# Performance work log

Hardware: AMD Instinct MI355X
Metric: run time of the kernel (lower is better)

The kernel has to match this reference:

```python
import jax, jax.numpy as jnp
import numpy as np

B = 131072
IN_C = 10
N = 512
HEAD_DIMS = [N, 128, 64, 32, 16, 1]
N_HEADS = 8


def _init_linear(key, fan_in, fan_out, batch=None):
    kw, kb = jax.random.split(key)
    shape_w = (fan_in, fan_out) if batch is None else (batch, fan_in, fan_out)
    shape_b = (fan_out,) if batch is None else (batch, fan_out)
    lim = 1.0 / np.sqrt(fan_in)
    W = jax.random.uniform(kw, shape_w, jnp.float32, -lim, lim)
    b = jax.random.uniform(kb, shape_b, jnp.float32, -lim, lim)
    return W, b


def setup_inputs() -> dict:
    key = jax.random.key(0)
    keys = jax.random.split(key, 10)
    x = jax.random.normal(keys[0], (B, IN_C), jnp.float32)
    W1, b1 = _init_linear(keys[1], 3 * IN_C, N)
    W2, b2 = _init_linear(keys[2], N, N)
    W3, b3 = _init_linear(keys[3], N, N - 3 * IN_C)
    W4, b4 = _init_linear(keys[4], N, N)
    inp = {"x": x, "W1": W1, "b1": b1, "W2": W2, "b2": b2,
           "W3": W3, "b3": b3, "W4": W4, "b4": b4}
    # 8 identical-shaped heads stacked into grouped weights [8, in, out]
    for i in range(5):
        HW, Hb = _init_linear(keys[5 + i], HEAD_DIMS[i], HEAD_DIMS[i + 1], batch=N_HEADS)
        inp[f"HW{i+1}"] = HW
        inp[f"Hb{i+1}"] = Hb
    return inp


def reference(x, W1, b1, W2, b2, W3, b3, W4, b4,
              HW1, Hb1, HW2, Hb2, HW3, Hb3, HW4, Hb4, HW5, Hb5):
    # backbone
    x_skip = jnp.concatenate([x, jnp.sin(x), jnp.cos(x)], axis=-1)  # [B, 3c]
    h = jax.nn.relu(x_skip @ W1 + b1)
    h = jax.nn.relu(h @ W2 + b2)
    h = h @ W3 + b3                                                  # [B, N-3c]
    h = jax.nn.relu(jnp.concatenate([h, x_skip], axis=1))            # [B, N]
    h = h @ W4 + b4  # NOTE: original discards the relu here (no assignment)
    # 8 heads as grouped batched GEMMs: y[g] = head_g(h)
    y = jax.nn.relu(jnp.einsum('bd,gde->gbe', h, HW1) + Hb1[:, None, :])
    y = jax.nn.relu(jnp.einsum('gbd,gde->gbe', y, HW2) + Hb2[:, None, :])
    y = jax.nn.relu(jnp.einsum('gbd,gde->gbe', y, HW3) + Hb3[:, None, :])
    y = jax.nn.relu(jnp.einsum('gbd,gde->gbe', y, HW4) + Hb4[:, None, :])
    y = jnp.einsum('gbd,gde->gbe', y, HW5) + Hb5[:, None, :]         # [8, B, 1]
    return jnp.transpose(y[..., 0])                                  # [B, 8]
```

## Files before the change

kernel.cpp:

```cpp
#include <hip/hip_runtime.h>
#include <hip/hip_bf16.h>

typedef short s16x8 __attribute__((ext_vector_type(8)));
typedef float f32x4 __attribute__((ext_vector_type(4)));
typedef unsigned short u16;
typedef unsigned int u32;

#define TB 64
#define NTHREADS 512

#define P_L1 0
#define P_L2 16384
#define P_L3 278528
#define P_L4 540672
#define P_H1 802816
#define P_H2 1327104
#define P_H3 1392640
#define P_H4 1409024
#define P_TOT 1413120

#define H_OFF   0
#define XS_OFF  65536
#define Y1_OFF  73728
#define LDS_BYTES 139264

__device__ __forceinline__ u16 f2bf(float v) {
  __hip_bfloat16 b = __float2bfloat16(v);
  return __builtin_bit_cast(u16, b);
}
__device__ __forceinline__ float bf2f(u16 u) {
  u32 x = ((u32)u) << 16;
  return __builtin_bit_cast(float, x);
}

template<int FN>
__device__ __forceinline__ void loadB(s16x8 (&b)[FN], const char* unit,
                                      int nCols, int bColBase, int kg, int l15) {
#pragma unroll
  for (int fj = 0; fj < FN; ++fj) {
    const int n = bColBase + fj * 16 + l15;
    b[fj] = *reinterpret_cast<const s16x8*>(unit + (kg * nCols + n) * 16);
  }
}

template<int FM, int FN>
__device__ __forceinline__ void mfma_step(
    const char* lds, int aOff, int aRB, int kByte, int mBase, int l15,
    const s16x8 (&b)[FN], f32x4 (&acc)[FM][FN]) {
  s16x8 a[FM];
#pragma unroll
  for (int fi = 0; fi < FM; ++fi) {
    const int m = mBase + fi * 16 + l15;
    a[fi] = *reinterpret_cast<const s16x8*>(
        lds + aOff + m * aRB + (kByte ^ (((m & 7) << 4) & (aRB - 1))));
  }
#pragma unroll
  for (int fi = 0; fi < FM; ++fi)
#pragma unroll
    for (int fj = 0; fj < FN; ++fj)
      acc[fi][fj] = __builtin_amdgcn_mfma_f32_16x16x32_bf16(a[fi], b[fj], acc[fi][fj], 0, 0, 0);
}

template<int FM, int FN, int KSTEPS>
__device__ __forceinline__ void gemm_reg(
    const char* lds, int aOff, int aRB, int aColBase, int mBase,
    const char* bGlob, int unitStride, int nCols, int bColBase,
    int kg, int l15, f32x4 (&acc)[FM][FN]) {
#pragma unroll
  for (int i = 0; i < FM; ++i)
#pragma unroll
    for (int j = 0; j < FN; ++j) { f32x4 z = {0.f,0.f,0.f,0.f}; acc[i][j] = z; }
  s16x8 bA[FN], bB[FN];
  loadB<FN>(bA, bGlob, nCols, bColBase, kg, l15);
#pragma unroll
  for (int ks = 0; ks < KSTEPS; ks += 2) {
    if (ks + 1 < KSTEPS)
      loadB<FN>(bB, bGlob + (size_t)(ks + 1) * unitStride, nCols, bColBase, kg, l15);
    mfma_step<FM, FN>(lds, aOff, aRB, (aColBase + ks * 32 + kg * 8) * 2,
                      mBase, l15, bA, acc);
    if (ks + 1 < KSTEPS) {
      if (ks + 2 < KSTEPS)
        loadB<FN>(bA, bGlob + (size_t)(ks + 2) * unitStride, nCols, bColBase, kg, l15);
      mfma_step<FM, FN>(lds, aOff, aRB, (aColBase + (ks + 1) * 32 + kg * 8) * 2,
                        mBase, l15, bB, acc);
    }
  }
}

__device__ __forceinline__ void epi_bb(char* lds, const f32x4 (&acc)[4][4],
    const float* bias, int biasLim, bool relu, bool concatXS, int tid)
{
  const int lane = tid & 63;
  const int l15 = lane & 15, rgrp = lane >> 4;
  const int wid = tid >> 6;
#pragma unroll
  for (int fj = 0; fj < 4; ++fj) {
    const int gc = wid * 64 + fj * 16 + l15;
    const float bv = (gc < biasLim) ? bias[gc] : 0.f;
#pragma unroll
    for (int fi = 0; fi < 4; ++fi) {
#pragma unroll
      for (int r = 0; r < 4; ++r) {
        const int m = fi * 16 + rgrp * 4 + r;
        float v = acc[fi][fj][r] + bv;
        if (relu) v = fmaxf(v, 0.f);
        u16 hv = f2bf(v);
        if (concatXS && gc >= 482) {
          const int c2 = gc - 482;
          const float xv = bf2f(*reinterpret_cast<const u16*>(
              lds + XS_OFF + m * 128 + ((c2 * 2) ^ ((m & 7) << 4))));
          hv = f2bf(fmaxf(xv, 0.f));
        }
        *reinterpret_cast<u16*>(lds + H_OFF + m * 1024 + ((gc * 2) ^ ((m & 7) << 4))) = hv;
      }
    }
  }
}

__global__ __launch_bounds__(256)
void prep_weights(const float* __restrict__ W1, const float* __restrict__ W2,
                  const float* __restrict__ W3, const float* __restrict__ W4,
                  const float* __restrict__ HW1, const float* __restrict__ HW2,
                  const float* __restrict__ HW3, const float* __restrict__ HW4,
                  u16* __restrict__ wp)
{
  for (int idx = blockIdx.x * blockDim.x + threadIdx.x; idx < P_TOT;
       idx += gridDim.x * blockDim.x) {
    float v;
    if (idx < P_L2) {
      const int e = idx;
      const int kg = e >> 12, n = (e >> 3) & 511, j = e & 7;
      const int k = kg * 8 + j;
      v = (k < 30) ? W1[k * 512 + n] : 0.f;
    } else if (idx < P_L3) {
      const int e = idx - P_L2;
      const int u = e >> 14, r = e & 16383;
      const int kg = r >> 12, n = (r >> 3) & 511, j = r & 7;
      const int k = u * 32 + kg * 8 + j;
      v = W2[k * 512 + n];
    } else if (idx < P_L4) {
      const int e = idx - P_L3;
      const int u = e >> 14, r = e & 16383;
      const int kg = r >> 12, n = (r >> 3) & 511, j = r & 7;
      const int k = u * 32 + kg * 8 + j;
      v = (n < 482) ? W3[k * 482 + n] : 0.f;
    } else if (idx < P_H1) {
      const int e = idx - P_L4;
      const int u = e >> 14, r = e & 16383;
      const int kg = r >> 12, n = (r >> 3) & 511, j = r & 7;
      const int k = u * 32 + kg * 8 + j;
      v = W4[k * 512 + n];
    } else if (idx < P_H2) {
      const int e = idx - P_H1;
      const int p = e >> 17, r = e & 131071;
      const int u = r >> 13, q = r & 8191;
      const int kg = q >> 11, n = (q >> 3) & 255, j = q & 7;
      const int k = u * 32 + kg * 8 + j;
      const int g = 2 * p + (n >> 7), col = n & 127;
      v = HW1[((size_t)g * 512 + k) * 128 + col];
    } else if (idx < P_H3) {
      const int e = idx - P_H2;
      const int p = e >> 14, r = e & 16383;
      const int u = r >> 12, q = r & 4095;
      const int kg = q >> 10, n = (q >> 3) & 127, j = q & 7;
      const int k = u * 32 + kg * 8 + j;
      const int g = 2 * p + (n >> 6), col = n & 63;
      v = HW2[((size_t)g * 128 + k) * 64 + col];
    } else if (idx < P_H4) {
      const int e = idx - P_H3;
      const int p = e >> 12, r = e & 4095;
      const int u = r >> 11, q = r & 2047;
      const int kg = q >> 9, n = (q >> 3) & 63, j = q & 7;
      const int k = u * 32 + kg * 8 + j;
      const int g = 2 * p + (n >> 5), col = n & 31;
      v = HW3[((size_t)g * 64 + k) * 32 + col];
    } else {
      const int e = idx - P_H4;
      const int p = e >> 10, q = e & 1023;
      const int kg = q >> 8, n = (q >> 3) & 31, j = q & 7;
      const int k = kg * 8 + j;
      const int g = 2 * p + (n >> 4), col = n & 15;
      v = HW4[((size_t)g * 32 + k) * 16 + col];
    }
    wp[idx] = f2bf(v);
  }
}

__global__ __launch_bounds__(NTHREADS, 2)
void fused_mlp(const float* __restrict__ x, const u16* __restrict__ wp,
               const float* __restrict__ b1, const float* __restrict__ b2,
               const float* __restrict__ b3, const float* __restrict__ b4,
               const float* __restrict__ Hb1, const float* __restrict__ Hb2,
               const float* __restrict__ Hb3, const float* __restrict__ Hb4,
               const float* __restrict__ hw5, const float* __restrict__ Hb5,
               float* __restrict__ out)
{
  extern __shared__ char lds[];
  const int tid = threadIdx.x;
  const int lane = tid & 63;
  const int l15 = lane & 15;
  const int rgrp = lane >> 4;
  const int kg = lane >> 4;
  const int wid = tid >> 6;
  const int row0 = blockIdx.x * TB;
  const char* wpB = reinterpret_cast<const char*>(wp);

  for (int i = tid; i < TB * 10; i += NTHREADS) {
    const int r = i / 10, c = i % 10;
    const float xv = x[(size_t)(row0 + r) * 10 + c];
    const int sw = (r & 7) << 4;
    char* rowp = lds + XS_OFF + r * 128;
    *reinterpret_cast<u16*>(rowp + ((c * 2) ^ sw)) = f2bf(xv);
    *reinterpret_cast<u16*>(rowp + (((c + 10) * 2) ^ sw)) = f2bf(__sinf(xv));
    *reinterpret_cast<u16*>(rowp + (((c + 20) * 2) ^ sw)) = f2bf(__cosf(xv));
  }
  for (int i = tid; i < TB * 2; i += NTHREADS) {
    const int r = i >> 1, c = 30 + (i & 1);
    *reinterpret_cast<u16*>(lds + XS_OFF + r * 128 + ((c * 2) ^ ((r & 7) << 4))) = 0;
  }
  __syncthreads();

  {
    f32x4 acc[4][4];
    gemm_reg<4, 4, 1>(lds, XS_OFF, 128, 0, 0,
                      wpB + (size_t)P_L1 * 2, 8192, 512, wid * 64, kg, l15, acc);
    epi_bb(lds, acc, b1, 512, true, false, tid);
    __syncthreads();
  }
  {
    f32x4 acc[4][4];
    gemm_reg<4, 4, 16>(lds, H_OFF, 1024, 0, 0,
                       wpB + (size_t)P_L2 * 2, 32768, 512, wid * 64, kg, l15, acc);
    __syncthreads();
    epi_bb(lds, acc, b2, 512, true, false, tid);
    __syncthreads();
  }
  {
    f32x4 acc[4][4];
    gemm_reg<4, 4, 16>(lds, H_OFF, 1024, 0, 0,
                       wpB + (size_t)P_L3 * 2, 32768, 512, wid * 64, kg, l15, acc);
    __syncthreads();
    epi_bb(lds, acc, b3, 482, true, true, tid);
    __syncthreads();
  }
  {
    f32x4 acc[4][4];
    gemm_reg<4, 4, 16>(lds, H_OFF, 1024, 0, 0,
                       wpB + (size_t)P_L4 * 2, 32768, 512, wid * 64, kg, l15, acc);
    __syncthreads();
    epi_bb(lds, acc, b4, 512, false, false, tid);
    __syncthreads();
  }

  {
    const int half = wid & 1;
    const int mB = half * 32;
    for (int grp = 0; grp < 2; ++grp) {
      const int g = grp * 4 + (wid >> 1);
      const int pair = g >> 1, side = g & 1;
      const int y1o = Y1_OFF + (g & 3) * 16384;
      const int scrOff = y1o + half * 8192;
      char* scr = lds + scrOff;

#pragma unroll
      for (int pass = 0; pass < 2; ++pass) {
        f32x4 acc[2][4];
        gemm_reg<2, 4, 16>(lds, H_OFF, 1024, 0, mB,
                           wpB + (size_t)P_H1 * 2 + (size_t)pair * 262144, 16384, 256,
                           side * 128 + pass * 64, kg, l15, acc);
#pragma unroll
        for (int fj = 0; fj < 4; ++fj) {
          const int c = pass * 64 + fj * 16 + l15;
          const float bv = Hb1[g * 128 + c];
#pragma unroll
          for (int fi = 0; fi < 2; ++fi)
#pragma unroll
            for (int r = 0; r < 4; ++r) {
              const int m = mB + fi * 16 + rgrp * 4 + r;
              const float v = fmaxf(acc[fi][fj][r] + bv, 0.f);
              *reinterpret_cast<u16*>(lds + y1o + m * 256 + ((c * 2) ^ ((m & 7) << 4))) = f2bf(v);
            }
        }
      }
      {
        f32x4 a2[2][4];
        gemm_reg<2, 4, 4>(lds, scrOff, 256, 0, 0,
                          wpB + (size_t)P_H2 * 2 + (size_t)pair * 32768, 8192, 128,
                          side * 64, kg, l15, a2);
#pragma unroll
        for (int fj = 0; fj < 4; ++fj) {
          const int c = fj * 16 + l15;
          const float bv = Hb2[g * 64 + c];
#pragma unroll
          for (int fi = 0; fi < 2; ++fi)
#pragma unroll
            for (int r = 0; r < 4; ++r) {
              const int rl = fi * 16 + rgrp * 4 + r;
              const float v = fmaxf(a2[fi][fj][r] + bv, 0.f);
              *reinterpret_cast<u16*>(scr + rl * 256 + ((c * 2) ^ ((rl & 7) << 4))) = f2bf(v);
            }
        }
      }
      {
        f32x4 a3[2][2];
        gemm_reg<2, 2, 2>(lds, scrOff, 256, 0, 0,
                          wpB + (size_t)P_H3 * 2 + (size_t)pair * 8192, 4096, 64,
                          side * 32, kg, l15, a3);
#pragma unroll
        for (int fj = 0; fj < 2; ++fj) {
          const int c = fj * 16 + l15;
          const float bv = Hb3[g * 32 + c];
#pragma unroll
          for (int fi = 0; fi < 2; ++fi)
#pragma unroll
            for (int r = 0; r < 4; ++r) {
              const int rl = fi * 16 + rgrp * 4 + r;
              const float v = fmaxf(a3[fi][fj][r] + bv, 0.f);
              *reinterpret_cast<u16*>(scr + rl * 256 + ((c * 2) ^ ((rl & 7) << 4))) = f2bf(v);
            }
        }
      }
      {
        f32x4 a4[2][1];
        gemm_reg<2, 1, 1>(lds, scrOff, 256, 0, 0,
                          wpB + (size_t)P_H4 * 2 + (size_t)pair * 2048, 2048, 32,
                          side * 16, kg, l15, a4);
        const int c = l15;
        const float bv = Hb4[g * 16 + c];
#pragma unroll
        for (int fi = 0; fi < 2; ++fi)
#pragma unroll
          for (int r = 0; r < 4; ++r) {
            const int rl = fi * 16 + rgrp * 4 + r;
            const float v = fmaxf(a4[fi][0][r] + bv, 0.f);
            *reinterpret_cast<u16*>(scr + rl * 256 + ((c * 2) ^ ((rl & 7) << 4))) = f2bf(v);
          }
      }
      {
        const int r = lane & 31, kh = lane >> 5;
        const s16x8 y4v = *reinterpret_cast<const s16x8*>(
            scr + r * 256 + ((kh * 16) ^ ((r & 7) << 4)));
        float partial = 0.f;
#pragma unroll
        for (int j = 0; j < 8; ++j)
          partial += bf2f((u16)y4v[j]) * hw5[g * 16 + kh * 8 + j];
        partial += __shfl_xor(partial, 32, 64);
        if (kh == 0)
          out[(size_t)(row0 + mB + r) * 8 + g] = Hb5[g] + partial;
      }
    }
  }
}

extern "C" void kernel_launch(void* const* d_in, const int* in_sizes, int n_in,
                              void* d_out, int out_size, void* d_ws, size_t ws_size,
                              hipStream_t stream) {
  (void)in_sizes; (void)n_in; (void)out_size; (void)ws_size;
  const float* x   = (const float*)d_in[0];
  const float* W1  = (const float*)d_in[1];
  const float* b1  = (const float*)d_in[2];
  const float* W2  = (const float*)d_in[3];
  const float* b2  = (const float*)d_in[4];
  const float* W3  = (const float*)d_in[5];
  const float* b3  = (const float*)d_in[6];
  const float* W4  = (const float*)d_in[7];
  const float* b4  = (const float*)d_in[8];
  const float* HW1 = (const float*)d_in[9];
  const float* Hb1 = (const float*)d_in[10];
  const float* HW2 = (const float*)d_in[11];
  const float* Hb2 = (const float*)d_in[12];
  const float* HW3 = (const float*)d_in[13];
  const float* Hb3 = (const float*)d_in[14];
  const float* HW4 = (const float*)d_in[15];
  const float* Hb4 = (const float*)d_in[16];
  const float* HW5 = (const float*)d_in[17];
  const float* Hb5 = (const float*)d_in[18];
  float* out = (float*)d_out;
  u16* wp = (u16*)d_ws;

  prep_weights<<<2048, 256, 0, stream>>>(W1, W2, W3, W4, HW1, HW2, HW3, HW4, wp);

  hipFuncSetAttribute((const void*)fused_mlp,
                      hipFuncAttributeMaxDynamicSharedMemorySize, LDS_BYTES);
  fused_mlp<<<131072 / TB, NTHREADS, LDS_BYTES, stream>>>(
      x, wp, b1, b2, b3, b4, Hb1, Hb2, Hb3, Hb4, HW5, Hb5, out);
}
```

Baseline: 427.7 us.

## Double-buffer activations in LDS and prefetch next layer's first weight tile

```diff
diff --git a/kernel.cpp b/kernel.cpp
--- a/kernel.cpp
+++ b/kernel.cpp
@@ -19,9 +19,9 @@
 #define P_H4 1409024
 #define P_TOT 1413120
 
-#define H_OFF   0
-#define XS_OFF  65536
-#define Y1_OFF  73728
+#define BUF0   0
+#define XS_OFF 65536
+#define BUF1   73728
 #define LDS_BYTES 139264
 
 __device__ __forceinline__ u16 f2bf(float v) {
@@ -62,16 +62,15 @@
 }
 
 template<int FM, int FN, int KSTEPS>
-__device__ __forceinline__ void gemm_reg(
+__device__ __forceinline__ void gemm_pre(
     const char* lds, int aOff, int aRB, int aColBase, int mBase,
     const char* bGlob, int unitStride, int nCols, int bColBase,
-    int kg, int l15, f32x4 (&acc)[FM][FN]) {
+    int kg, int l15, f32x4 (&acc)[FM][FN], s16x8 (&bA)[FN]) {
 #pragma unroll
   for (int i = 0; i < FM; ++i)
 #pragma unroll
     for (int j = 0; j < FN; ++j) { f32x4 z = {0.f,0.f,0.f,0.f}; acc[i][j] = z; }
-  s16x8 bA[FN], bB[FN];
-  loadB<FN>(bA, bGlob, nCols, bColBase, kg, l15);
+  s16x8 bB[FN];
 #pragma unroll
   for (int ks = 0; ks < KSTEPS; ks += 2) {
     if (ks + 1 < KSTEPS)
@@ -87,8 +86,19 @@
   }
 }
 
+template<int FM, int FN, int KSTEPS>
+__device__ __forceinline__ void gemm_reg(
+    const char* lds, int aOff, int aRB, int aColBase, int mBase,
+    const char* bGlob, int unitStride, int nCols, int bColBase,
+    int kg, int l15, f32x4 (&acc)[FM][FN]) {
+  s16x8 bA[FN];
+  loadB<FN>(bA, bGlob, nCols, bColBase, kg, l15);
+  gemm_pre<FM, FN, KSTEPS>(lds, aOff, aRB, aColBase, mBase, bGlob, unitStride,
+                           nCols, bColBase, kg, l15, acc, bA);
+}
+
 __device__ __forceinline__ void epi_bb(char* lds, const f32x4 (&acc)[4][4],
-    const float* bias, int biasLim, bool relu, bool concatXS, int tid)
+    int outOff, const float* bias, int biasLim, bool relu, bool concatXS, int tid)
 {
   const int lane = tid & 63;
   const int l15 = lane & 15, rgrp = lane >> 4;
@@ -111,7 +121,7 @@
               lds + XS_OFF + m * 128 + ((c2 * 2) ^ ((m & 7) << 4))));
           hv = f2bf(fmaxf(xv, 0.f));
         }
-        *reinterpret_cast<u16*>(lds + H_OFF + m * 1024 + ((gc * 2) ^ ((m & 7) << 4))) = hv;
+        *reinterpret_cast<u16*>(lds + outOff + m * 1024 + ((gc * 2) ^ ((m & 7) << 4))) = hv;
       }
     }
   }
@@ -205,6 +215,9 @@
   const int row0 = blockIdx.x * TB;
   const char* wpB = reinterpret_cast<const char*>(wp);
 
+  s16x8 bPre[4];
+  loadB<4>(bPre, wpB + (size_t)P_L1 * 2, 512, wid * 64, kg, l15);
+
   for (int i = tid; i < TB * 10; i += NTHREADS) {
     const int r = i / 10, c = i % 10;
     const float xv = x[(size_t)(row0 + r) * 10 + c];
@@ -222,33 +235,39 @@
 
   {
     f32x4 acc[4][4];
-    gemm_reg<4, 4, 1>(lds, XS_OFF, 128, 0, 0,
-                      wpB + (size_t)P_L1 * 2, 8192, 512, wid * 64, kg, l15, acc);
-    epi_bb(lds, acc, b1, 512, true, false, tid);
+    gemm_pre<4, 4, 1>(lds, XS_OFF, 128, 0, 0,
+                      wpB + (size_t)P_L1 * 2, 8192, 512, wid * 64, kg, l15, acc, bPre);
+    loadB<4>(bPre, wpB + (size_t)P_L2 * 2, 512, wid * 64, kg, l15);
+    epi_bb(lds, acc, BUF0, b1, 512, true, false, tid);
     __syncthreads();
   }
   {
     f32x4 acc[4][4];
-    gemm_reg<4, 4, 16>(lds, H_OFF, 1024, 0, 0,
-                       wpB + (size_t)P_L2 * 2, 32768, 512, wid * 64, kg, l15, acc);
-    __syncthreads();
-    epi_bb(lds, acc, b2, 512, true, false, tid);
+    gemm_pre<4, 4, 16>(lds, BUF0, 1024, 0, 0,
+                       wpB + (size_t)P_L2 * 2, 32768, 512, wid * 64, kg, l15, acc, bPre);
+    loadB<4>(bPre, wpB + (size_t)P_L3 * 2, 512, wid * 64, kg, l15);
+    epi_bb(lds, acc, BUF1, b2, 512, true, false, tid);
     __syncthreads();
   }
   {
     f32x4 acc[4][4];
-    gemm_reg<4, 4, 16>(lds, H_OFF, 1024, 0, 0,
-                       wpB + (size_t)P_L3 * 2, 32768, 512, wid * 64, kg, l15, acc);
+    gemm_pre<4, 4, 16>(lds, BUF1, 1024, 0, 0,
+                       wpB + (size_t)P_L3 * 2, 32768, 512, wid * 64, kg, l15, acc, bPre);
+    loadB<4>(bPre, wpB + (size_t)P_L4 * 2, 512, wid * 64, kg, l15);
+    epi_bb(lds, acc, BUF0, b3, 482, true, true, tid);
     __syncthreads();
-    epi_bb(lds, acc, b3, 482, true, true, tid);
-    __syncthreads();
-  }
+  }
+  const int h4 = wid >> 1, chalf = wid & 1;
   {
     f32x4 acc[4][4];
-    gemm_reg<4, 4, 16>(lds, H_OFF, 1024, 0, 0,
-                       wpB + (size_t)P_L4 * 2, 32768, 512, wid * 64, kg, l15, acc);
-    __syncthreads();
-    epi_bb(lds, acc, b4, 512, false, false, tid);
+    gemm_pre<4, 4, 16>(lds, BUF0, 1024, 0, 0,
+                       wpB + (size_t)P_L4 * 2, 32768, 512, wid * 64, kg, l15, acc, bPre);
+    {
+      const int g1 = h4, pair1 = g1 >> 1, side1 = g1 & 1;
+      loadB<4>(bPre, wpB + (size_t)P_H1 * 2 + (size_t)pair1 * 262144, 256,
+               side1 * 128 + chalf * 64, kg, l15);
+    }
+    epi_bb(lds, acc, BUF1, b4, 512, false, false, tid);
     __syncthreads();
   }
 
@@ -256,37 +275,46 @@
     const int half = wid & 1;
     const int mB = half * 32;
     for (int grp = 0; grp < 2; ++grp) {
-      const int g = grp * 4 + (wid >> 1);
+      const int g = grp * 4 + h4;
       const int pair = g >> 1, side = g & 1;
-      const int y1o = Y1_OFF + (g & 3) * 16384;
-      const int scrOff = y1o + half * 8192;
-      char* scr = lds + scrOff;
-
-#pragma unroll
-      for (int pass = 0; pass < 2; ++pass) {
-        f32x4 acc[2][4];
-        gemm_reg<2, 4, 16>(lds, H_OFF, 1024, 0, mB,
+      if (grp) {
+        loadB<4>(bPre, wpB + (size_t)P_H1 * 2 + (size_t)pair * 262144, 256,
+                 side * 128 + chalf * 64, kg, l15);
+        __syncthreads();
+      }
+
+      {
+        f32x4 acc[4][4];
+        gemm_pre<4, 4, 16>(lds, BUF1, 1024, 0, 0,
                            wpB + (size_t)P_H1 * 2 + (size_t)pair * 262144, 16384, 256,
-                           side * 128 + pass * 64, kg, l15, acc);
+                           side * 128 + chalf * 64, kg, l15, acc, bPre);
+        loadB<4>(bPre, wpB + (size_t)P_H2 * 2 + (size_t)pair * 32768, 128,
+                 side * 64, kg, l15);
+        const int y1o = (g & 3) * 16384;
 #pragma unroll
         for (int fj = 0; fj < 4; ++fj) {
-          const int c = pass * 64 + fj * 16 + l15;
+          const int c = chalf * 64 + fj * 16 + l15;
           const float bv = Hb1[g * 128 + c];
 #pragma unroll
-          for (int fi = 0; fi < 2; ++fi)
+          for (int fi = 0; fi < 4; ++fi)
 #pragma unroll
             for (int r = 0; r < 4; ++r) {
-              const int m = mB + fi * 16 + rgrp * 4 + r;
+              const int m = fi * 16 + rgrp * 4 + r;
               const float v = fmaxf(acc[fi][fj][r] + bv, 0.f);
               *reinterpret_cast<u16*>(lds + y1o + m * 256 + ((c * 2) ^ ((m & 7) << 4))) = f2bf(v);
             }
         }
       }
+      __syncthreads();
+
+      const int scrOff = (g & 3) * 16384 + half * 8192;
+      char* scr = lds + scrOff;
+
       {
         f32x4 a2[2][4];
-        gemm_reg<2, 4, 4>(lds, scrOff, 256, 0, 0,
+        gemm_pre<2, 4, 4>(lds, scrOff, 256, 0, 0,
                           wpB + (size_t)P_H2 * 2 + (size_t)pair * 32768, 8192, 128,
-                          side * 64, kg, l15, a2);
+                          side * 64, kg, l15, a2, bPre);
 #pragma unroll
         for (int fj = 0; fj < 4; ++fj) {
           const int c = fj * 16 + l15;
```

Result: slower. 552.4 us (+29.2%).
